# Optimization experiments

Hardware: AMD Instinct MI355X
Metric: run time of the kernel (lower is better)

## Reference

```python
import jax, jax.numpy as jnp
import numpy as np

NEG_SLOPE = 0.2
EPS = 1e-16


def _add_self_loops(edge_index, num_nodes):
    loop = jnp.arange(num_nodes, dtype=edge_index.dtype)
    return jnp.concatenate([edge_index, jnp.stack([loop, loop])], axis=1)


def gat_conv(x, edge_index, W, a_src, a_dst, b, concat):
    """PyG-style GATConv: gather -> attention logits -> segment softmax -> scatter-add."""
    N = x.shape[0]
    H, C = a_src.shape
    xl = (x @ W).reshape(N, H, C)                       # [N,H,C]
    alpha_src = (xl * a_src[None]).sum(-1)              # [N,H]
    alpha_dst = (xl * a_dst[None]).sum(-1)              # [N,H]
    src, dst = edge_index[0], edge_index[1]
    alpha = jax.nn.leaky_relu(alpha_src[src] + alpha_dst[dst], NEG_SLOPE)  # [E,H]
    amax = jax.ops.segment_max(alpha, dst, num_segments=N)
    amax = jnp.where(jnp.isfinite(amax), amax, 0.0)
    ea = jnp.exp(alpha - amax[dst])
    denom = jax.ops.segment_sum(ea, dst, num_segments=N)
    attn = ea / (denom[dst] + EPS)                      # [E,H]
    msg = xl[src] * attn[:, :, None]                    # [E,H,C]
    out = jax.ops.segment_sum(msg, dst, num_segments=N)  # [N,H,C]
    out = out.reshape(N, H * C) if concat else out.mean(axis=1)
    return out + b


def setup_inputs() -> dict:
    key = jax.random.key(0)
    ks = jax.random.split(key, 9)
    N, F, E, H, C, NC = 100000, 128, 1600000, 8, 8, 40
    s = lambda fan: 1.0 / np.sqrt(fan)
    return {
        "x": jax.random.normal(ks[0], (N, F), dtype=jnp.float32),
        "edge_index": jax.random.randint(ks[1], (2, E), 0, N, dtype=jnp.int64),
        "W1": jax.random.normal(ks[2], (F, H * C), dtype=jnp.float32) * s(F),
        "a_src1": jax.random.normal(ks[3], (H, C), dtype=jnp.float32) * s(C),
        "a_dst1": jax.random.normal(ks[4], (H, C), dtype=jnp.float32) * s(C),
        "b1": jnp.zeros((H * C,), dtype=jnp.float32),
        "W2": jax.random.normal(ks[5], (H * C, NC), dtype=jnp.float32) * s(H * C),
        "a_src2": jax.random.normal(ks[6], (1, NC), dtype=jnp.float32) * s(NC),
        "a_dst2": jax.random.normal(ks[7], (1, NC), dtype=jnp.float32) * s(NC),
        "b2": jnp.zeros((NC,), dtype=jnp.float32),
    }


def reference(x, edge_index, W1, a_src1, a_dst1, b1, W2, a_src2, a_dst2, b2):
    N = x.shape[0]
    ei = _add_self_loops(edge_index, N)
    h = gat_conv(x, ei, W1, a_src1, a_dst1, b1, concat=True)   # [N,64]
    h = jax.nn.elu(h)
    out = gat_conv(h, ei, W2, a_src2, a_dst2, b2, concat=True)  # [N,nclass]
    return out
```

## Files before the change

kernel.cpp:

```cpp
#include <hip/hip_runtime.h>
#include <math.h>

#define NEG_SLOPE 0.2f
#define GAT_EPS 1e-16f
#define LOG2E 1.44269504088896340736f

#define CH   2048
#define NBK  512

__device__ __forceinline__ unsigned pack_bf16(float a, float b) {
    unsigned ua = __float_as_uint(a);
    unsigned ub = __float_as_uint(b);
    ua = (ua + 0x8000u) >> 16;
    ub = (ub + 0x8000u) & 0xffff0000u;
    return ua | ub;
}
__device__ __forceinline__ float bf_lo(unsigned pk) {
    return __uint_as_float(pk << 16);
}
__device__ __forceinline__ float bf_hi(unsigned pk) {
    return __uint_as_float(pk & 0xffff0000u);
}


__global__ __launch_bounds__(256) void k_off_a(
    const int* __restrict__ cnt, int* __restrict__ off,
    int* __restrict__ tot, int NCHv)
{
    __shared__ int sm[256];
    int b = blockIdx.x;
    int t = threadIdx.x;
    int carry = 0;
    for (int c0 = 0; c0 < NCHv; c0 += 256) {
        int c = c0 + t;
        int v = (c < NCHv) ? cnt[c * NBK + b] : 0;
        sm[t] = v;
        __syncthreads();
        for (int o = 1; o < 256; o <<= 1) {
            int add = (t >= o) ? sm[t - o] : 0;
            __syncthreads();
            sm[t] += add;
            __syncthreads();
        }
        if (c < NCHv) off[c * NBK + b] = carry + sm[t] - v;
        carry += sm[255];
        __syncthreads();
    }
    if (t == 0) tot[b] = carry;
}

__global__ __launch_bounds__(256) void k_place(
    const int* __restrict__ ei, int E, int N, int shift,
    const int* __restrict__ off, const int* __restrict__ tot,
    unsigned* __restrict__ bslab)
{
    __shared__ int cur[NBK];
    __shared__ int ps[256];
    int c = blockIdx.x;
    int t = threadIdx.x;
    int carry = 0;
    for (int b0 = 0; b0 < NBK; b0 += 256) {
        int v = tot[b0 + t];
        ps[t] = v;
        __syncthreads();
        for (int o = 1; o < 256; o <<= 1) {
            int u = (t >= o) ? ps[t - o] : 0;
            __syncthreads();
            ps[t] += u;
            __syncthreads();
        }
        cur[b0 + t] = carry + ps[t] - v + off[(size_t)c * NBK + b0 + t];
        carry += ps[255];
        __syncthreads();
    }
    __syncthreads();

    int Etot = E + N;
    int base = c * CH;
    int lim = min(base + CH, Etot);
    int mask = (1 << shift) - 1;
    for (int e = base + t; e < lim; e += 256) {
        int s, d;
        if (e < E) { s = ei[e]; d = ei[E + e]; }
        else       { s = e - E; d = s; }
        int b = d >> shift;
        int pos = atomicAdd(&cur[b], 1);
        bslab[pos] = (unsigned)s | ((unsigned)(d & mask) << 17);
    }
}

__global__ __launch_bounds__(256) void k_csr2(
    const int* __restrict__ tot, const unsigned* __restrict__ bslab,
    int shift, int* __restrict__ row_ptr, int* __restrict__ csr_src,
    int N, int Etot)
{
    __shared__ int sdeg[1024];
    __shared__ int scur[1024];
    __shared__ int ps[256];
    __shared__ int bb[NBK + 1];
    int b = blockIdx.x;
    int tid = threadIdx.x;

    int carry = 0;
    for (int b0 = 0; b0 < NBK; b0 += 256) {
        int v = tot[b0 + tid];
        ps[tid] = v;
        __syncthreads();
        for (int o = 1; o < 256; o <<= 1) {
            int u = (tid >= o) ? ps[tid - o] : 0;
            __syncthreads();
            ps[tid] += u;
            __syncthreads();
        }
        bb[b0 + tid] = carry + ps[tid] - v;
        carry += ps[255];
        __syncthreads();
    }
    if (tid == 0) bb[NBK] = carry;
    __syncthreads();

    int beg = bb[b], end = bb[b + 1];
    int nodes = 1 << shift;
    int node0 = b << shift;
    for (int i = tid; i < nodes; i += 256) sdeg[i] = 0;
    __syncthreads();
    for (int i = beg + tid; i < end; i += 256)
        atomicAdd(&sdeg[bslab[i] >> 17], 1);
    __syncthreads();
    int per = (nodes + 255) / 256;
    int mybase = tid * per;
    int sum = 0;
    for (int j = 0; j < per; j++) sum += sdeg[mybase + j];
    ps[tid] = sum;
    __syncthreads();
    int v0 = ps[tid];
    for (int o = 1; o < 256; o <<= 1) {
        int v = (tid >= o) ? ps[tid - o] : 0;
        __syncthreads();
        ps[tid] += v;
        __syncthreads();
    }
    int run = ps[tid] - v0;
    for (int j = 0; j < per; j++) {
        int i = mybase + j;
        int dgi = sdeg[i];
        scur[i] = beg + run;
        int node = node0 + i;
        if (node < N) row_ptr[node] = beg + run;
        run += dgi;
    }
    if (b == 0 && tid == 0) row_ptr[N] = Etot;
    __syncthreads();
    for (int i = beg + tid; i < end; i += 256) {
        unsigned w = bslab[i];
        int pos = atomicAdd(&scur[w >> 17], 1);
        csr_src[pos] = (int)(w & 0x1FFFFu);
    }
}

__device__ __forceinline__ void emit_node1(
    const float* acc, int n, int q, int c0,
    const float* asrc, const float* adst,
    unsigned* __restrict__ xl1b, float* __restrict__ as1,
    float* __restrict__ ad1)
{
    uint4 pk0, pk1;
    pk0.x = pack_bf16(acc[0], acc[1]);  pk0.y = pack_bf16(acc[2], acc[3]);
    pk0.z = pack_bf16(acc[4], acc[5]);  pk0.w = pack_bf16(acc[6], acc[7]);
    pk1.x = pack_bf16(acc[8], acc[9]);  pk1.y = pack_bf16(acc[10], acc[11]);
    pk1.z = pack_bf16(acc[12], acc[13]); pk1.w = pack_bf16(acc[14], acc[15]);
    uint4* xo = (uint4*)(xl1b + (size_t)n * 32 + q * 8);
    xo[0] = pk0;
    xo[1] = pk1;
#pragma unroll
    for (int hh = 0; hh < 2; hh++) {
        float s = 0.0f, t = 0.0f;
#pragma unroll
        for (int c = 0; c < 8; c++) {
            s = fmaf(acc[hh * 8 + c], asrc[c0 + hh * 8 + c], s);
            t = fmaf(acc[hh * 8 + c], adst[c0 + hh * 8 + c], t);
        }
        as1[(size_t)n * 8 + 2 * q + hh] = s * LOG2E;
        ad1[(size_t)n * 8 + 2 * q + hh] = t * LOG2E;
    }
}

__global__ __launch_bounds__(256) void k_gemm1(
    const float* __restrict__ x, const float* __restrict__ W1,
    const float* __restrict__ a_src1, const float* __restrict__ a_dst1,
    unsigned* __restrict__ xl1b, float* __restrict__ as1,
    float* __restrict__ ad1, int N, int F,
    const int* __restrict__ ei, int E, int shift, int NCHv,
    int* __restrict__ cnt)
{
    __shared__ float Ws[128 * 64];
    __shared__ float asrc[64];
    __shared__ float adst[64];
    __shared__ int hist[NBK];

    if (blockIdx.x < NCHv) {
        for (int i = threadIdx.x; i < NBK; i += 256) hist[i] = 0;
        __syncthreads();
        int Etot = E + N;
        int base = blockIdx.x * CH;
        int lim = min(base + CH, Etot);
        for (int e = base + threadIdx.x; e < lim; e += 256) {
            int d = (e < E) ? ei[E + e] : (e - E);
            atomicAdd(&hist[d >> shift], 1);
        }
        __syncthreads();
        for (int i = threadIdx.x; i < NBK; i += 256)
            cnt[(size_t)blockIdx.x * NBK + i] = hist[i];
    }
    if (blockIdx.x * 256 >= N) return;

    for (int i = threadIdx.x; i < F * 64; i += 256) Ws[i] = W1[i];
    if (threadIdx.x < 64) {
        asrc[threadIdx.x] = a_src1[threadIdx.x];
        adst[threadIdx.x] = a_dst1[threadIdx.x];
    }
    __syncthreads();

    int q = threadIdx.x & 3;
    int n0 = blockIdx.x * 256 + (threadIdx.x >> 2) * 4;
    if (n0 >= N) return;
    int c0 = q * 16;
    int n1 = min(n0 + 1, N - 1);
    int n2 = min(n0 + 2, N - 1);
    int n3 = min(n0 + 3, N - 1);

    float acc0[16], acc1[16], acc2[16], acc3[16];
#pragma unroll
    for (int c = 0; c < 16; c++) { acc0[c]=0.f; acc1[c]=0.f; acc2[c]=0.f; acc3[c]=0.f; }

    const float4* xr0 = (const float4*)(x + (size_t)n0 * F);
    const float4* xr1 = (const float4*)(x + (size_t)n1 * F);
    const float4* xr2 = (const float4*)(x + (size_t)n2 * F);
    const float4* xr3 = (const float4*)(x + (size_t)n3 * F);

#define GEMM1_ROW(comp, ridx)                                        \
    { const float* w = &Ws[(k4 * 4 + ridx) * 64 + c0];               \
      _Pragma("unroll")                                              \
      for (int c = 0; c < 16; c++) {                                 \
          float wc = w[c];                                           \
          acc0[c] = fmaf(xv0.comp, wc, acc0[c]);                     \
          acc1[c] = fmaf(xv1.comp, wc, acc1[c]);                     \
          acc2[c] = fmaf(xv2.comp, wc, acc2[c]);                     \
          acc3[c] = fmaf(xv3.comp, wc, acc3[c]); } }

    for (int k4 = 0; k4 < F / 4; k4++) {
        float4 xv0 = xr0[k4];
        float4 xv1 = xr1[k4];
        float4 xv2 = xr2[k4];
        float4 xv3 = xr3[k4];
        GEMM1_ROW(x, 0)
        GEMM1_ROW(y, 1)
        GEMM1_ROW(z, 2)
        GEMM1_ROW(w, 3)
    }
#undef GEMM1_ROW

    emit_node1(acc0, n0, q, c0, asrc, adst, xl1b, as1, ad1);
    if (n0 + 1 < N) emit_node1(acc1, n0 + 1, q, c0, asrc, adst, xl1b, as1, ad1);
    if (n0 + 2 < N) emit_node1(acc2, n0 + 2, q, c0, asrc, adst, xl1b, as1, ad1);
    if (n0 + 3 < N) emit_node1(acc3, n0 + 3, q, c0, asrc, adst, xl1b, as1, ad1);
}

__global__ __launch_bounds__(256) void k_agg1(
    const int* __restrict__ row_ptr, const int* __restrict__ csr_src,
    const float* __restrict__ as1, const float* __restrict__ ad1,
    const unsigned* __restrict__ xl1b, const float* __restrict__ b1,
    float* __restrict__ h1, int N)
{
    int d = blockIdx.x * 8 + ((threadIdx.x >> 6) << 1) + ((threadIdx.x >> 5) & 1);
    if (d >= N) return;
    int lane = threadIdx.x & 31;
    int g = lane >> 3;
    int l = lane & 7;

    int beg = row_ptr[d], end = row_ptr[d + 1];
    float adh = ad1[(size_t)d * 8 + l];

    float ax[8];
#pragma unroll
    for (int j = 0; j < 8; j++) ax[j] = 0.f;
    float den = 0.f;

    int i = beg + g;
    for (; i + 4 < end; i += 8) {
        int s0 = csr_src[i];
        int s1 = csr_src[i + 4];
        size_t q0 = (size_t)s0 * 8 + l;
        size_t q1 = (size_t)s1 * 8 + l;
        float al0 = as1[q0] + adh;
        float al1 = as1[q1] + adh;
        uint4 k0 = *(const uint4*)(xl1b + (q0 << 2));
        uint4 k1 = *(const uint4*)(xl1b + (q1 << 2));
        al0 = fmaxf(al0, NEG_SLOPE * al0);
        al1 = fmaxf(al1, NEG_SLOPE * al1);
        float e0 = __builtin_amdgcn_exp2f(al0);
        float e1 = __builtin_amdgcn_exp2f(al1);
        ax[0] = fmaf(e0, bf_lo(k0.x), ax[0]);
        ax[1] = fmaf(e0, bf_hi(k0.x), ax[1]);
        ax[2] = fmaf(e0, bf_lo(k0.y), ax[2]);
        ax[3] = fmaf(e0, bf_hi(k0.y), ax[3]);
        ax[4] = fmaf(e0, bf_lo(k0.z), ax[4]);
        ax[5] = fmaf(e0, bf_hi(k0.z), ax[5]);
        ax[6] = fmaf(e0, bf_lo(k0.w), ax[6]);
        ax[7] = fmaf(e0, bf_hi(k0.w), ax[7]);
        ax[0] = fmaf(e1, bf_lo(k1.x), ax[0]);
        ax[1] = fmaf(e1, bf_hi(k1.x), ax[1]);
        ax[2] = fmaf(e1, bf_lo(k1.y), ax[2]);
        ax[3] = fmaf(e1, bf_hi(k1.y), ax[3]);
        ax[4] = fmaf(e1, bf_lo(k1.z), ax[4]);
        ax[5] = fmaf(e1, bf_hi(k1.z), ax[5]);
        ax[6] = fmaf(e1, bf_lo(k1.w), ax[6]);
        ax[7] = fmaf(e1, bf_hi(k1.w), ax[7]);
        den += e0 + e1;
    }
    if (i < end) {
        int s0 = csr_src[i];
        size_t q0 = (size_t)s0 * 8 + l;
        float al0 = as1[q0] + adh;
        uint4 k0 = *(const uint4*)(xl1b + (q0 << 2));
        al0 = fmaxf(al0, NEG_SLOPE * al0);
        float e0 = __builtin_amdgcn_exp2f(al0);
        ax[0] = fmaf(e0, bf_lo(k0.x), ax[0]);
        ax[1] = fmaf(e0, bf_hi(k0.x), ax[1]);
        ax[2] = fmaf(e0, bf_lo(k0.y), ax[2]);
        ax[3] = fmaf(e0, bf_hi(k0.y), ax[3]);
        ax[4] = fmaf(e0, bf_lo(k0.z), ax[4]);
        ax[5] = fmaf(e0, bf_hi(k0.z), ax[5]);
        ax[6] = fmaf(e0, bf_lo(k0.w), ax[6]);
        ax[7] = fmaf(e0, bf_hi(k0.w), ax[7]);
        den += e0;
    }

#pragma unroll
    for (int m = 8; m < 32; m <<= 1) {
#pragma unroll
        for (int j = 0; j < 8; j++) ax[j] += __shfl_xor(ax[j], m);
        den += __shfl_xor(den, m);
    }

    if (g == 0) {
        float inv = __builtin_amdgcn_rcpf(den + GAT_EPS);
        const float4* bb = (const float4*)(b1 + l * 8);
        float4 b0 = bb[0], b1v = bb[1];
        float4 o0, o1;
        float v;
        v = fmaf(ax[0], inv, b0.x);  o0.x = v > 0.f ? v : __expf(v) - 1.f;
        v = fmaf(ax[1], inv, b0.y);  o0.y = v > 0.f ? v : __expf(v) - 1.f;
        v = fmaf(ax[2], inv, b0.z);  o0.z = v > 0.f ? v : __expf(v) - 1.f;
        v = fmaf(ax[3], inv, b0.w);  o0.w = v > 0.f ? v : __expf(v) - 1.f;
        v = fmaf(ax[4], inv, b1v.x); o1.x = v > 0.f ? v : __expf(v) - 1.f;
        v = fmaf(ax[5], inv, b1v.y); o1.y = v > 0.f ? v : __expf(v) - 1.f;
        v = fmaf(ax[6], inv, b1v.z); o1.z = v > 0.f ? v : __expf(v) - 1.f;
        v = fmaf(ax[7], inv, b1v.w); o1.w = v > 0.f ? v : __expf(v) - 1.f;
        float4* op = (float4*)(h1 + (size_t)d * 64 + l * 8);
        op[0] = o0;
        op[1] = o1;
    }
}

__global__ __launch_bounds__(256) void k_node2(
    const float* __restrict__ h1, const float* __restrict__ W2,
    const float* __restrict__ a_src2, const float* __restrict__ a_dst2,
    unsigned* __restrict__ xl2b, float* __restrict__ ad2, int N)
{
    __shared__ float Ws[64 * 40];
    __shared__ float a2s[40];
    __shared__ float a2d[40];
    for (int i = threadIdx.x; i < 64 * 40; i += 256) Ws[i] = W2[i];
    if (threadIdx.x < 40) {
        a2s[threadIdx.x] = a_src2[threadIdx.x];
        a2d[threadIdx.x] = a_dst2[threadIdx.x];
    }
    __syncthreads();

    int q = threadIdx.x & 1;
    int n0 = blockIdx.x * 256 + (threadIdx.x >> 1) * 2;
    if (n0 >= N) return;
    int c0 = q * 20;
    int n1 = min(n0 + 1, N - 1);

    float o0[20], o1[20];
#pragma unroll
    for (int j = 0; j < 20; j++) { o0[j] = 0.f; o1[j] = 0.f; }

    const float4* hr0 = (const float4*)(h1 + (size_t)n0 * 64);
    const float4* hr1 = (const float4*)(h1 + (size_t)n1 * 64);

#define NODE2_ROW(comp, ridx)                                        \
    { const float* w = &Ws[(k4 * 4 + ridx) * 40 + c0];               \
      _Pragma("unroll")                                              \
      for (int j = 0; j < 20; j++) {                                 \
          float wj = w[j];                                           \
          o0[j] = fmaf(ha.comp, wj, o0[j]);                          \
          o1[j] = fmaf(hb.comp, wj, o1[j]); } }

    for (int k4 = 0; k4 < 16; k4++) {
        float4 ha = hr0[k4];
        float4 hb = hr1[k4];
        NODE2_ROW(x, 0)
        NODE2_ROW(y, 1)
        NODE2_ROW(z, 2)
        NODE2_ROW(w, 3)
    }
#undef NODE2_ROW

    float s0 = 0.f, t0 = 0.f, s1 = 0.f, t1 = 0.f;
#pragma unroll
    for (int j = 0; j < 20; j++) {
        s0 = fmaf(o0[j], a2s[c0 + j], s0);
        t0 = fmaf(o0[j], a2d[c0 + j], t0);
        s1 = fmaf(o1[j], a2s[c0 + j], s1);
        t1 = fmaf(o1[j], a2d[c0 + j], t1);
    }
    s0 += __shfl_xor(s0, 1);
    t0 += __shfl_xor(t0, 1);
    s1 += __shfl_xor(s1, 1);
    t1 += __shfl_xor(t1, 1);
    if (q == 0) {
        xl2b[(size_t)n0 * 24 + 20] = __float_as_uint(s0 * LOG2E);
        ad2[n0] = t0 * LOG2E;
        if (n0 + 1 < N) {
            xl2b[(size_t)(n0 + 1) * 24 + 20] = __float_as_uint(s1 * LOG2E);
            ad2[n0 + 1] = t1 * LOG2E;
        }
    }

    unsigned* xo0 = xl2b + (size_t)n0 * 24 + q * 10;
#pragma unroll
    for (int p = 0; p < 10; p++) xo0[p] = pack_bf16(o0[2 * p], o0[2 * p + 1]);
    if (n0 + 1 < N) {
        unsigned* xo1 = xl2b + (size_t)(n0 + 1) * 24 + q * 10;
#pragma unroll
        for (int p = 0; p < 10; p++) xo1[p] = pack_bf16(o1[2 * p], o1[2 * p + 1]);
    }
}

__global__ __launch_bounds__(256) void k_agg2(
    const int* __restrict__ row_ptr, const int* __restrict__ csr_src,
    const float* __restrict__ ad2,
    const unsigned* __restrict__ xl2b, const float* __restrict__ b2,
    float* __restrict__ out, int N)
{
    int d = blockIdx.x * 8 + ((threadIdx.x >> 6) << 1) + ((threadIdx.x >> 5) & 1);
    if (d >= N) return;
    int lane = threadIdx.x & 31;
    int g = lane >> 3;
    int l = lane & 7;
    if (l >= 5) return;

    int beg = row_ptr[d], end = row_ptr[d + 1];
    float add = ad2[d];

    float ax[8];
#pragma unroll
    for (int j = 0; j < 8; j++) ax[j] = 0.f;
    float den = 0.f;

    int i = beg + g;
    for (; i + 4 < end; i += 8) {
        int s0 = csr_src[i];
        int s1 = csr_src[i + 4];
        const unsigned* r0 = xl2b + (size_t)s0 * 24;
        const unsigned* r1 = xl2b + (size_t)s1 * 24;
        float al0 = __uint_as_float(r0[20]) + add;
        float al1 = __uint_as_float(r1[20]) + add;
        uint4 k0 = *(const uint4*)(r0 + l * 4);
        uint4 k1 = *(const uint4*)(r1 + l * 4);
        al0 = fmaxf(al0, NEG_SLOPE * al0);
        al1 = fmaxf(al1, NEG_SLOPE * al1);
        float e0 = __builtin_amdgcn_exp2f(al0);
        float e1 = __builtin_amdgcn_exp2f(al1);
        ax[0] = fmaf(e0, bf_lo(k0.x), ax[0]);
        ax[1] = fmaf(e0, bf_hi(k0.x), ax[1]);
        ax[2] = fmaf(e0, bf_lo(k0.y), ax[2]);
        ax[3] = fmaf(e0, bf_hi(k0.y), ax[3]);
        ax[4] = fmaf(e0, bf_lo(k0.z), ax[4]);
        ax[5] = fmaf(e0, bf_hi(k0.z), ax[5]);
        ax[6] = fmaf(e0, bf_lo(k0.w), ax[6]);
        ax[7] = fmaf(e0, bf_hi(k0.w), ax[7]);
        ax[0] = fmaf(e1, bf_lo(k1.x), ax[0]);
        ax[1] = fmaf(e1, bf_hi(k1.x), ax[1]);
        ax[2] = fmaf(e1, bf_lo(k1.y), ax[2]);
        ax[3] = fmaf(e1, bf_hi(k1.y), ax[3]);
        ax[4] = fmaf(e1, bf_lo(k1.z), ax[4]);
        ax[5] = fmaf(e1, bf_hi(k1.z), ax[5]);
        ax[6] = fmaf(e1, bf_lo(k1.w), ax[6]);
        ax[7] = fmaf(e1, bf_hi(k1.w), ax[7]);
        den += e0 + e1;
    }
    if (i < end) {
        int s0 = csr_src[i];
        const unsigned* r0 = xl2b + (size_t)s0 * 24;
        float al0 = __uint_as_float(r0[20]) + add;
        uint4 k0 = *(const uint4*)(r0 + l * 4);
        al0 = fmaxf(al0, NEG_SLOPE * al0);
        float e0 = __builtin_amdgcn_exp2f(al0);
        ax[0] = fmaf(e0, bf_lo(k0.x), ax[0]);
        ax[1] = fmaf(e0, bf_hi(k0.x), ax[1]);
        ax[2] = fmaf(e0, bf_lo(k0.y), ax[2]);
        ax[3] = fmaf(e0, bf_hi(k0.y), ax[3]);
        ax[4] = fmaf(e0, bf_lo(k0.z), ax[4]);
        ax[5] = fmaf(e0, bf_hi(k0.z), ax[5]);
        ax[6] = fmaf(e0, bf_lo(k0.w), ax[6]);
        ax[7] = fmaf(e0, bf_hi(k0.w), ax[7]);
        den += e0;
    }

#pragma unroll
    for (int m = 8; m < 32; m <<= 1) {
#pragma unroll
        for (int j = 0; j < 8; j++) ax[j] += __shfl_xor(ax[j], m);
        den += __shfl_xor(den, m);
    }

    if (g == 0) {
        float inv = __builtin_amdgcn_rcpf(den + GAT_EPS);
        float* op = out + (size_t)d * 40 + l * 8;
        const float* bb = b2 + l * 8;
#pragma unroll
        for (int j = 0; j < 8; j++) op[j] = fmaf(ax[j], inv, bb[j]);
    }
}

extern "C" void kernel_launch(void* const* d_in, const int* in_sizes, int n_in,
                              void* d_out, int out_size, void* d_ws, size_t ws_size,
                              hipStream_t stream) {
    const float* x      = (const float*)d_in[0];
    const int*   ei     = (const int*)d_in[1];
    const float* W1     = (const float*)d_in[2];
    const float* a_src1 = (const float*)d_in[3];
    const float* a_dst1 = (const float*)d_in[4];
    const float* b1     = (const float*)d_in[5];
    const float* W2     = (const float*)d_in[6];
    const float* a_src2 = (const float*)d_in[7];
    const float* a_dst2 = (const float*)d_in[8];
    const float* b2     = (const float*)d_in[9];

    int F = in_sizes[2] / 64;
    int N = in_sizes[0] / F;
    int E = in_sizes[1] / 2;
    int Etot = E + N;
    int NCHv = (Etot + CH - 1) / CH;
    int shift = 8;
    while (((N - 1) >> shift) >= NBK) shift++;

    unsigned* xl1b    = (unsigned*)d_ws;
    float*    h1      = (float*)(xl1b + (size_t)N * 32);
    float*    as1     = h1 + (size_t)N * 64;
    float*    ad1     = as1 + (size_t)N * 8;
    int*      row_ptr = (int*)(ad1 + (size_t)N * 8);
    int*      csr_src = row_ptr + (N + 1);
    unsigned* bslab   = (unsigned*)(csr_src + Etot);
    int*      cnt     = (int*)h1;
    int*      off     = cnt + (size_t)NCHv * NBK;
    int*      tot     = off + (size_t)NCHv * NBK;
    unsigned* xl2b    = xl1b;
    float*    ad2     = ad1;

    int gridG1 = (N + 255) / 256;
    if (gridG1 < NCHv) gridG1 = NCHv;
    k_gemm1<<<gridG1, 256, 0, stream>>>(x, W1, a_src1, a_dst1,
                                        xl1b, as1, ad1, N, F,
                                        ei, E, shift, NCHv, cnt);

    k_off_a<<<NBK, 256, 0, stream>>>(cnt, off, tot, NCHv);
    k_place<<<NCHv, 256, 0, stream>>>(ei, E, N, shift, off, tot, bslab);
    k_csr2 <<<NBK, 256, 0, stream>>>(tot, bslab, shift,
                                     row_ptr, csr_src, N, Etot);

    k_agg1 <<<(N + 7) / 8, 256, 0, stream>>>(row_ptr, csr_src, as1, ad1,
                                             xl1b, b1, h1, N);

    k_node2<<<(N + 255) / 256, 256, 0, stream>>>(h1, W2, a_src2, a_dst2,
                                                 xl2b, ad2, N);
    k_agg2 <<<(N + 7) / 8, 256, 0, stream>>>(row_ptr, csr_src, ad2,
                                             xl2b, b2, (float*)d_out, N);
}
```

Baseline: 293.0 us.

## Rework offset scan, prefetch GEMM1 inputs, and split agg1 into two launches

The offset-scan kernel now handles 8 buckets per block. It stages all chunk counts in shared memory and does a two-level serial/parallel scan, which replaces the many-barrier Hillis-Steele loop. The GEMM1 inner loop gets a two-stage register prefetch of the x rows to hide global load latency. The first aggregation launch is split into two half-range launches, which adds launch overhead with no clear benefit. MAXCH caps the chunk count in shared memory, so a larger NCHv would overflow.

```diff
diff --git a/kernel.cpp b/kernel.cpp
--- a/kernel.cpp
+++ b/kernel.cpp
@@ -7,6 +7,7 @@
 
 #define CH   2048
 #define NBK  512
+#define MAXCH 864
 
 __device__ __forceinline__ unsigned pack_bf16(float a, float b) {
     unsigned ua = __float_as_uint(a);
@@ -27,26 +28,37 @@
     const int* __restrict__ cnt, int* __restrict__ off,
     int* __restrict__ tot, int NCHv)
 {
-    __shared__ int sm[256];
-    int b = blockIdx.x;
+    __shared__ int st[8][MAXCH];
+    __shared__ int psum[8][33];
+    int b0 = blockIdx.x * 8;
     int t = threadIdx.x;
-    int carry = 0;
-    for (int c0 = 0; c0 < NCHv; c0 += 256) {
-        int c = c0 + t;
-        int v = (c < NCHv) ? cnt[c * NBK + b] : 0;
-        sm[t] = v;
-        __syncthreads();
-        for (int o = 1; o < 256; o <<= 1) {
-            int add = (t >= o) ? sm[t - o] : 0;
-            __syncthreads();
-            sm[t] += add;
-            __syncthreads();
-        }
-        if (c < NCHv) off[c * NBK + b] = carry + sm[t] - v;
-        carry += sm[255];
-        __syncthreads();
-    }
-    if (t == 0) tot[b] = carry;
+    for (int idx = t; idx < NCHv * 8; idx += 256) {
+        int bl = idx & 7, c = idx >> 3;
+        st[bl][c] = cnt[(size_t)c * NBK + b0 + bl];
+    }
+    __syncthreads();
+    int bl = t >> 5, j = t & 31;
+    int per = (NCHv + 31) / 32;
+    int cbeg = j * per;
+    int cend = min(cbeg + per, NCHv);
+    int s = 0;
+    for (int c = cbeg; c < cend; c++) s += st[bl][c];
+    psum[bl][j] = s;
+    __syncthreads();
+    if (j == 0) {
+        int run = 0;
+        for (int k = 0; k < 32; k++) { int v = psum[bl][k]; psum[bl][k] = run; run += v; }
+        psum[bl][32] = run;
+    }
+    __syncthreads();
+    int run = psum[bl][j];
+    for (int c = cbeg; c < cend; c++) { int v = st[bl][c]; st[bl][c] = run; run += v; }
+    __syncthreads();
+    for (int idx = t; idx < NCHv * 8; idx += 256) {
+        int blw = idx & 7, c = idx >> 3;
+        off[(size_t)c * NBK + b0 + blw] = st[blw][c];
+    }
+    if (j == 0) tot[b0 + bl] = psum[bl][32];
 }
 
 __global__ __launch_bounds__(256) void k_place(
@@ -248,15 +260,19 @@
           acc2[c] = fmaf(xv2.comp, wc, acc2[c]);                     \
           acc3[c] = fmaf(xv3.comp, wc, acc3[c]); } }
 
-    for (int k4 = 0; k4 < F / 4; k4++) {
-        float4 xv0 = xr0[k4];
-        float4 xv1 = xr1[k4];
-        float4 xv2 = xr2[k4];
-        float4 xv3 = xr3[k4];
+    int K4 = F / 4;
+    float4 xv0 = xr0[0], xv1 = xr1[0], xv2 = xr2[0], xv3 = xr3[0];
+    float4 nx0 = xr0[1], nx1 = xr1[1], nx2 = xr2[1], nx3 = xr3[1];
+    for (int k4 = 0; k4 < K4; k4++) {
+        float4 fx0 = xv0, fx1 = xv1, fx2 = xv2, fx3 = xv3;
+        int kn = k4 + 2;
+        if (kn < K4) { fx0 = xr0[kn]; fx1 = xr1[kn]; fx2 = xr2[kn]; fx3 = xr3[kn]; }
         GEMM1_ROW(x, 0)
         GEMM1_ROW(y, 1)
         GEMM1_ROW(z, 2)
         GEMM1_ROW(w, 3)
+        xv0 = nx0; xv1 = nx1; xv2 = nx2; xv3 = nx3;
+        nx0 = fx0; nx1 = fx1; nx2 = fx2; nx3 = fx3;
     }
 #undef GEMM1_ROW
 
@@ -270,10 +286,10 @@
     const int* __restrict__ row_ptr, const int* __restrict__ csr_src,
     const float* __restrict__ as1, const float* __restrict__ ad1,
     const unsigned* __restrict__ xl1b, const float* __restrict__ b1,
-    float* __restrict__ h1, int N)
-{
-    int d = blockIdx.x * 8 + ((threadIdx.x >> 6) << 1) + ((threadIdx.x >> 5) & 1);
-    if (d >= N) return;
+    float* __restrict__ h1, int d0, int dend)
+{
+    int d = d0 + blockIdx.x * 8 + ((threadIdx.x >> 6) << 1) + ((threadIdx.x >> 5) & 1);
+    if (d >= dend) return;
     int lane = threadIdx.x & 31;
     int g = lane >> 3;
     int l = lane & 7;
@@ -568,13 +584,16 @@
                                         xl1b, as1, ad1, N, F,
                                         ei, E, shift, NCHv, cnt);
 
-    k_off_a<<<NBK, 256, 0, stream>>>(cnt, off, tot, NCHv);
+    k_off_a<<<NBK / 8, 256, 0, stream>>>(cnt, off, tot, NCHv);
     k_place<<<NCHv, 256, 0, stream>>>(ei, E, N, shift, off, tot, bslab);
     k_csr2 <<<NBK, 256, 0, stream>>>(tot, bslab, shift,
                                      row_ptr, csr_src, N, Etot);
 
-    k_agg1 <<<(N + 7) / 8, 256, 0, stream>>>(row_ptr, csr_src, as1, ad1,
-                                             xl1b, b1, h1, N);
+    int N1 = (N / 2) & ~7;
+    k_agg1 <<<(N1 + 7) / 8, 256, 0, stream>>>(row_ptr, csr_src, as1, ad1,
+                                              xl1b, b1, h1, 0, N1);
+    k_agg1 <<<((N - N1) + 7) / 8, 256, 0, stream>>>(row_ptr, csr_src, as1, ad1,
+                                                    xl1b, b1, h1, N1, N);
 
     k_node2<<<(N + 255) / 256, 256, 0, stream>>>(h1, W2, a_src2, a_dst2,
                                                  xl2b, ad2, N);
```

New measurement: 302.5 us. 3.2% more time.
